# Kernel optimization log

Measured on AMD Instinct MI355X. Metric: run time of the kernel, lower is better.

Reference implementation:

```python
import jax, jax.numpy as jnp
import numpy as np
import math


def _conv2d(x, w, b):
    # 3x3, stride 1, pad 1, NCHW / OIHW
    y = jax.lax.conv_general_dilated(x, w, (1, 1), ((1, 1), (1, 1)),
                                     dimension_numbers=('NCHW', 'OIHW', 'NCHW'))
    return y + b[None, :, None, None]


def _avgpool2(x):
    B, C, H, W = x.shape
    return x.reshape(B, C, H // 2, 2, W // 2, 2).mean(axis=(3, 5))


def setup_inputs() -> dict:
    key = jax.random.key(0)
    ks = jax.random.split(key, 12)
    B, H, W = 8, 512, 512
    x = jax.random.uniform(ks[0], (B, 3, H, W), dtype=jnp.float32)

    def conv_w(k, o, i):
        return jax.random.normal(k, (o, i, 3, 3), jnp.float32) / jnp.sqrt(jnp.float32(i * 9))

    def lin_w(k, o, i):
        return jax.random.normal(k, (o, i), jnp.float32) / jnp.sqrt(jnp.float32(i))

    return {
        'x': x,
        'w1': conv_w(ks[1], 16, 6),  'b1': jnp.zeros((16,), jnp.float32),
        'w2': conv_w(ks[2], 32, 16), 'b2': jnp.zeros((32,), jnp.float32),
        'w3': conv_w(ks[3], 64, 32), 'b3': jnp.zeros((64,), jnp.float32),
        'fw1': lin_w(ks[4], 256, 64),  'fb1': jnp.zeros((256,), jnp.float32),
        'fw2': lin_w(ks[5], 100, 256), 'fb2': jnp.zeros((100,), jnp.float32),
    }


def reference(x, w1, b1, w2, b2, w3, b3, fw1, fb1, fw2, fb2):
    B, C, H, W = x.shape
    # radial distance from image center (torch.meshgrid default = 'ij')
    a, b = jnp.meshgrid(jnp.arange(H), jnp.arange(W), indexing='ij')
    dist = jnp.sqrt((a - H / 2) ** 2 + (b - W / 2) ** 2).astype(jnp.float32)
    max_radius = math.sqrt(H * H + W * W) / 2

    xf = jnp.fft.fftn(x, axes=(-1, -2))
    # torch.fft.fftshift with no dim shifts ALL axes (incl. B, C); jnp matches.
    xf = jnp.fft.fftshift(xf)
    x_mag = jnp.log10(jnp.abs(xf) + 1)

    fi = jnp.concatenate([x, x_mag], axis=1)  # [B,6,H,W]
    y = jax.nn.relu(_conv2d(fi, w1, b1))
    y = _avgpool2(y)
    y = jax.nn.relu(_conv2d(y, w2, b2))
    y = _avgpool2(y)
    y = _conv2d(y, w3, b3)
    y = y.mean(axis=(2, 3))  # AdaptiveAvgPool2d((1,1)) -> [B,64]
    # note: NO activation between the two FC layers in the original
    value_set = jax.nn.leaky_relu((y @ fw1.T + fb1) @ fw2.T + fb2, 0.01)  # [B,100]

    # 100 radial ring bins; replace the 100-iter where-loop with bucketize+gather
    radius_set = max_radius * (jnp.arange(100, dtype=jnp.float32) + 1.0) * 0.01
    # bin i: radius_set[i-1] < dist <= radius_set[i]  ==  searchsorted left
    bin_idx = jnp.clip(jnp.searchsorted(radius_set, dist, side='left'), 0, 99)  # [H,W]
    fq_mask = value_set[:, bin_idx]  # [B,H,W] gather, same math as sum of ring masks

    low = xf * fq_mask[:, None, :, :]
    low = jnp.fft.ifftshift(low)
    low = jnp.fft.ifftn(low, axes=(-1, -2))
    lowpass = jnp.clip(low.real, 0.0, 1.0)
    return lowpass, fq_mask, value_set
```

## Files before the change

kernel.cpp:

```cpp
#include <hip/hip_runtime.h>
#include <math.h>

#define NPIX 262144
#define FSTR 513

typedef __attribute__((ext_vector_type(2))) float v2f;


__device__ __forceinline__ int brev9(int i) { return (int)(__brev((unsigned)i) >> 23); }

__device__ __forceinline__ void wave_lds_fence() {
  asm volatile("s_waitcnt lgkmcnt(0)" ::: "memory");
}

__device__ __forceinline__ void init_tw(float* twr, float* twi, int t) {
  if (t < 256) {
    float ang = -3.14159265358979323846f * (float)t / 256.0f;
    float s, c;
    sincosf(ang, &s, &c);
    twr[t] = c; twi[t] = s;
  }
}

template<bool FWD>
__device__ __forceinline__ void fft512x8(float* __restrict__ sr, float* __restrict__ si,
                                         const float* __restrict__ twr,
                                         const float* __restrict__ twi, int t) {
  const int c  = t >> 5;
  const int tq = t & 31;
  float* cr = sr + c * FSTR;
  float* ci = si + c * FSTR;
  #pragma unroll
  for (int sp = 0; sp < 4; sp++) {
    const int s = 2 * sp;
    const int h = 1 << s;
    if (sp == 0) __syncthreads(); else wave_lds_fence();
    #pragma unroll
    for (int m = 0; m < 4; m++) {
      int q = tq + 32 * m;
      int j = q & (h - 1);
      int base = ((q >> s) << (s + 2)) | j;
      int i1 = j << (8 - s);
      int i2 = j << (7 - s);
      float w1r = twr[i1], w1i = FWD ? twi[i1] : -twi[i1];
      float w2r = twr[i2], w2i = FWD ? twi[i2] : -twi[i2];
      float ar = cr[base],         ai = ci[base];
      float br = cr[base + h],     bi = ci[base + h];
      float c2r = cr[base + 2*h],  c2i = ci[base + 2*h];
      float dr = cr[base + 3*h],   di = ci[base + 3*h];
      float wbr = br * w1r - bi * w1i, wbi = br * w1i + bi * w1r;
      float wdr = dr * w1r - di * w1i, wdi = dr * w1i + di * w1r;
      float t0r = ar + wbr,  t0i = ai + wbi;
      float t1r = ar - wbr,  t1i = ai - wbi;
      float t2r = c2r + wdr, t2i = c2i + wdi;
      float t3r = c2r - wdr, t3i = c2i - wdi;
      float u2r = t2r * w2r - t2i * w2i, u2i = t2r * w2i + t2i * w2r;
      float v3r = t3r * w2r - t3i * w2i, v3i = t3r * w2i + t3i * w2r;
      float u3r = FWD ? v3i : -v3i;
      float u3i = FWD ? -v3r : v3r;
      cr[base]         = t0r + u2r;  ci[base]         = t0i + u2i;
      cr[base + 2*h]   = t0r - u2r;  ci[base + 2*h]   = t0i - u2i;
      cr[base + h]     = t1r + u3r;  ci[base + h]     = t1i + u3i;
      cr[base + 3*h]   = t1r - u3r;  ci[base + 3*h]   = t1i - u3i;
    }
  }
  wave_lds_fence();
  #pragma unroll
  for (int m = 0; m < 8; m++) {
    int k = tq + 32 * m;
    float wr = twr[k], wi = FWD ? twi[k] : -twi[k];
    float vr = cr[k + 256], vi = ci[k + 256];
    float tr = vr * wr - vi * wi;
    float ti = vr * wi + vi * wr;
    float ur = cr[k], ui = ci[k];
    cr[k] = ur + tr;        ci[k] = ui + ti;
    cr[k + 256] = ur - tr;  ci[k + 256] = ui - ti;
  }
  __syncthreads();
}

__device__ __forceinline__ void pair_src(int p, int& ia, int& ib) {
  if (p < 8) { ia = 3 * p; ib = 3 * p + 1; }
  else { int k = p - 8; ia = 6 * k + 2; ib = 6 * k + 5; }
}

__global__ __launch_bounds__(256) void k_fft_rows(const float* __restrict__ x,
                                                  float2* __restrict__ xf) {
  __shared__ float sr[8 * FSTR], si[8 * FSTR], twr[256], twi[256];
  int t = threadIdx.x;
  int p = blockIdx.x >> 6;
  int r0 = (blockIdx.x & 63) << 3;
  init_tw(twr, twi, t);
  int ia, ib;
  pair_src(p, ia, ib);
  const float4* pa = (const float4*)(x + (size_t)ia * NPIX + (size_t)r0 * 512);
  const float4* pb = (const float4*)(x + (size_t)ib * NPIX + (size_t)r0 * 512);
  for (int e = t; e < 1024; e += 256) {
    int row = e >> 7, w = e & 127;
    float4 fa = pa[e];
    float4 fb = pb[e];
    float* cr = sr + row * FSTR;
    float* ci = si + row * FSTR;
    int pc = 4 * w;
    cr[brev9(pc)]     = fa.x;  ci[brev9(pc)]     = fb.x;
    cr[brev9(pc + 1)] = fa.y;  ci[brev9(pc + 1)] = fb.y;
    cr[brev9(pc + 2)] = fa.z;  ci[brev9(pc + 2)] = fb.z;
    cr[brev9(pc + 3)] = fa.w;  ci[brev9(pc + 3)] = fb.w;
  }
  fft512x8<true>(sr, si, twr, twi, t);
  float4* q4 = (float4*)(xf + (size_t)p * NPIX + (size_t)r0 * 512);
  for (int e = t; e < 2048; e += 256) {
    int row = e >> 8, u = e & 255;
    const float* cr = sr + row * FSTR;
    const float* ci = si + row * FSTR;
    q4[e] = make_float4(cr[2 * u], ci[2 * u], cr[2 * u + 1], ci[2 * u + 1]);
  }
}

__global__ __launch_bounds__(256) void k_fft_cols(float2* __restrict__ xf) {
  __shared__ float sr[8 * FSTR], si[8 * FSTR], twr[256], twi[256];
  int t = threadIdx.x;
  int p = blockIdx.x >> 6;
  int c0 = (blockIdx.x & 63) << 3;
  init_tw(twr, twi, t);
  float2* base = xf + (size_t)p * NPIX + c0;
  const int q = t & 3;
  const int j = (t >> 2) & 15;
  const int w = t >> 6;
  #pragma unroll
  for (int it = 0; it < 8; it++) {
    int row = 32 * j + 4 * it + w;
    float4 f = *(const float4*)(base + (size_t)row * 512 + 2 * q);
    int rr = brev9(row);
    sr[(2 * q) * FSTR + rr]     = f.x;  si[(2 * q) * FSTR + rr]     = f.y;
    sr[(2 * q + 1) * FSTR + rr] = f.z;  si[(2 * q + 1) * FSTR + rr] = f.w;
  }
  fft512x8<true>(sr, si, twr, twi, t);
  const int rg = t >> 2;
  #pragma unroll
  for (int it = 0; it < 8; it++) {
    int row = 64 * it + rg;
    float a0 = sr[(2 * q) * FSTR + row],     b0 = si[(2 * q) * FSTR + row];
    float a1 = sr[(2 * q + 1) * FSTR + row], b1 = si[(2 * q + 1) * FSTR + row];
    *(float4*)(base + (size_t)row * 512 + 2 * q) = make_float4(a0, b0, a1, b1);
  }
}

__global__ __launch_bounds__(256) void k_xmag(const float2* __restrict__ xf,
                                              float* __restrict__ xmag) {
  int t = threadIdx.x;
  int p = blockIdx.x >> 6;
  int r0 = (blockIdx.x & 63) << 3;
  int da, db;
  if (p < 8) {
    int bs = (p + 4) & 7;
    da = bs * 3 + 1;
    db = bs * 3 + 2;
  } else {
    int k = p - 8;
    da = ((2 * k + 4) & 7) * 3;
    db = ((2 * k + 5) & 7) * 3;
  }
  const float2* Z = xf + (size_t)p * NPIX;
  float* A = xmag + (size_t)da * NPIX;
  float* B = xmag + (size_t)db * NPIX;
  for (int e = t; e < 2048; e += 256) {
    int row = r0 + (e >> 8);
    int c0 = (e & 255) * 2;
    float4 z01 = *(const float4*)(Z + (size_t)row * 512 + c0);
    int mr = (512 - row) & 511;
    float2 zm0 = Z[(size_t)mr * 512 + ((512 - c0) & 511)];
    float2 zm1 = Z[(size_t)mr * 512 + (511 - c0)];
    float ar0 = 0.5f * (z01.x + zm0.x), ai0 = 0.5f * (z01.y - zm0.y);
    float br0 = 0.5f * (z01.x - zm0.x), bi0 = 0.5f * (z01.y + zm0.y);
    float ar1 = 0.5f * (z01.z + zm1.x), ai1 = 0.5f * (z01.w - zm1.y);
    float br1 = 0.5f * (z01.z - zm1.x), bi1 = 0.5f * (z01.w + zm1.y);
    float ma0 = log10f(sqrtf(ar0 * ar0 + ai0 * ai0) + 1.0f);
    float ma1 = log10f(sqrtf(ar1 * ar1 + ai1 * ai1) + 1.0f);
    float mb0 = log10f(sqrtf(br0 * br0 + bi0 * bi0) + 1.0f);
    float mb1 = log10f(sqrtf(br1 * br1 + bi1 * bi1) + 1.0f);
    size_t off = (size_t)(row ^ 256) * 512 + (c0 ^ 256);
    *(float2*)(A + off) = make_float2(ma0, ma1);
    *(float2*)(B + off) = make_float2(mb0, mb1);
  }
}

__global__ __launch_bounds__(256) void k_conv1(const float* __restrict__ x,
                                               const float* __restrict__ xmag,
                                               const float* __restrict__ w1,
                                               const float* __restrict__ b1,
                                               float* __restrict__ out) {
  __shared__ float tile[2][18 * 132 + 8];
  const int t = threadIdx.x;
  const int tx = t & 31, ty = t >> 5;
  const int PC0 = blockIdx.x * 64;
  const int PR0 = blockIdx.y * 8;
  const int b  = blockIdx.z >> 1;
  const int og = (blockIdx.z & 1) * 8;
  const int R0 = PR0 * 2 - 1;
  const int C0 = PC0 * 2 - 1;

  int li[10], gi[10];
  bool okf[10];
  #pragma unroll
  for (int k = 0; k < 10; k++) {
    int e = t + 256 * k;
    bool valid = e < 2340;
    int i = e / 130, j = e - i * 130;
    int rr = R0 + i, cc = C0 + j;
    bool ok = valid && ((unsigned)rr < 512u) && ((unsigned)cc < 512u);
    li[k] = valid ? (i * 132 + j) : (18 * 132);
    gi[k] = ok ? (rr * 512 + cc) : 0;
    okf[k] = ok;
  }

  v2f acc[8][4];
  #pragma unroll
  for (int o = 0; o < 8; o++)
    #pragma unroll
    for (int q = 0; q < 4; q++) acc[o][q] = (v2f){0.0f, 0.0f};

  const float* xb = x + (size_t)(b * 3) * NPIX;
  const float* mb = xmag + (size_t)(b * 3) * NPIX;

  float ld[10];
  #pragma unroll
  for (int k = 0; k < 10; k++) ld[k] = okf[k] ? xb[gi[k]] : 0.0f;
  #pragma unroll
  for (int k = 0; k < 10; k++) tile[0][li[k]] = ld[k];
  __syncthreads();

  for (int ic = 0; ic < 6; ic++) {
    if (ic < 5) {
      const float* sn = (ic + 1 < 3) ? (xb + (size_t)(ic + 1) * NPIX)
                                     : (mb + (size_t)(ic - 2) * NPIX);
      #pragma unroll
      for (int k = 0; k < 10; k++) ld[k] = okf[k] ? sn[gi[k]] : 0.0f;
    }
    const float* cur = tile[ic & 1];
    float patch[4][6];
    #pragma unroll
    for (int dy = 0; dy < 4; dy++) {
      const float* rp = cur + (2 * ty + dy) * 132 + 4 * tx;
      float4 f = *(const float4*)rp;
      float2 g = *(const float2*)(rp + 4);
      patch[dy][0] = f.x; patch[dy][1] = f.y; patch[dy][2] = f.z;
      patch[dy][3] = f.w; patch[dy][4] = g.x; patch[dy][5] = g.y;
    }
    v2f pr[4][5];
    #pragma unroll
    for (int dy = 0; dy < 4; dy++)
      #pragma unroll
      for (int s = 0; s < 5; s++)
        pr[dy][s] = (v2f){patch[dy][s], patch[dy][s + 1]};
    #pragma unroll
    for (int o = 0; o < 8; o++) {
      const float* wk = w1 + (size_t)((og + o) * 6 + ic) * 9;
      #pragma unroll
      for (int dy = 0; dy < 3; dy++)
        #pragma unroll
        for (int kc = 0; kc < 3; kc++) {
          float kw = wk[dy * 3 + kc];
          v2f wv = (v2f){kw, kw};
          acc[o][0] += wv * pr[dy][kc];
          acc[o][1] += wv * pr[dy][kc + 2];
          acc[o][2] += wv * pr[dy + 1][kc];
          acc[o][3] += wv * pr[dy + 1][kc + 2];
        }
    }
    if (ic < 5) {
      float* nxt = tile[(ic + 1) & 1];
      #pragma unroll
      for (int k = 0; k < 10; k++) nxt[li[k]] = ld[k];
      __syncthreads();
    }
  }
  #pragma unroll
  for (int o = 0; o < 8; o++) {
    float bias = b1[og + o];
    float p0 = fmaxf(acc[o][0].x + bias, 0.0f) + fmaxf(acc[o][0].y + bias, 0.0f)
             + fmaxf(acc[o][2].x + bias, 0.0f) + fmaxf(acc[o][2].y + bias, 0.0f);
    float p1 = fmaxf(acc[o][1].x + bias, 0.0f) + fmaxf(acc[o][1].y + bias, 0.0f)
             + fmaxf(acc[o][3].x + bias, 0.0f) + fmaxf(acc[o][3].y + bias, 0.0f);
    float2* q = (float2*)(out + ((size_t)(b * 16 + og + o) * 256 + PR0 + ty) * 256 + PC0 + 2 * tx);
    *q = make_float2(p0 * 0.25f, p1 * 0.25f);
  }
}

__global__ __launch_bounds__(256) void k_conv2(const float* __restrict__ in,
                                               const float* __restrict__ w2,
                                               const float* __restrict__ b2,
                                               float* __restrict__ S) {
  __shared__ float tile[2][18 * 68 + 8];
  __shared__ float wsum[4][8];
  const int t = threadIdx.x;
  const int tx = t & 31, ty = t >> 5;
  const int bx = blockIdx.x, by = blockIdx.y;
  const int PC0 = bx * 32;
  const int PR0 = by * 8;
  const int b  = blockIdx.z >> 2;
  const int og = (blockIdx.z & 3) * 8;
  const int R0 = PR0 * 2 - 1;
  const int C0 = PC0 * 2 - 1;

  int li[5], gi[5];
  bool okf[5];
  #pragma unroll
  for (int k = 0; k < 5; k++) {
    int e = t + 256 * k;
    bool valid = e < 1188;
    int i = e / 66, j = e - 66 * i;
    int rr = R0 + i, cc = C0 + j;
    bool ok = valid && ((unsigned)rr < 256u) && ((unsigned)cc < 256u);
    li[k] = valid ? (i * 68 + j) : (18 * 68);
    gi[k] = ok ? (rr * 256 + cc) : 0;
    okf[k] = ok;
  }

  v2f acc[8][2];
  #pragma unroll
  for (int o = 0; o < 8; o++) {
    acc[o][0] = (v2f){0.0f, 0.0f};
    acc[o][1] = (v2f){0.0f, 0.0f};
  }

  const float* inb = in + (size_t)(b * 16) * 65536;

  float ld[5];
  #pragma unroll
  for (int k = 0; k < 5; k++) ld[k] = okf[k] ? inb[gi[k]] : 0.0f;
  #pragma unroll
  for (int k = 0; k < 5; k++) tile[0][li[k]] = ld[k];
  __syncthreads();

  for (int ic = 0; ic < 16; ic++) {
    if (ic < 15) {
      const float* sn = inb + (size_t)(ic + 1) * 65536;
      #pragma unroll
      for (int k = 0; k < 5; k++) ld[k] = okf[k] ? sn[gi[k]] : 0.0f;
    }
    const float* cur = tile[ic & 1];
    float patch[4][4];
    #pragma unroll
    for (int dy = 0; dy < 4; dy++) {
      const float* rp = cur + (2 * ty + dy) * 68 + 2 * tx;
      float2 f0 = *(const float2*)rp;
      float2 f1 = *(const float2*)(rp + 2);
      patch[dy][0] = f0.x; patch[dy][1] = f0.y;
      patch[dy][2] = f1.x; patch[dy][3] = f1.y;
    }
    v2f pr[4][3];
    #pragma unroll
    for (int dy = 0; dy < 4; dy++) {
      pr[dy][0] = (v2f){patch[dy][0], patch[dy][1]};
      pr[dy][1] = (v2f){patch[dy][1], patch[dy][2]};
      pr[dy][2] = (v2f){patch[dy][2], patch[dy][3]};
    }
    #pragma unroll
    for (int o = 0; o < 8; o++) {
      const float* wk = w2 + (size_t)((og + o) * 16 + ic) * 9;
      #pragma unroll
      for (int dy = 0; dy < 3; dy++)
        #pragma unroll
        for (int kc = 0; kc < 3; kc++) {
          float kw = wk[dy * 3 + kc];
          v2f wv = (v2f){kw, kw};
          acc[o][0] += wv * pr[dy][kc];
          acc[o][1] += wv * pr[dy + 1][kc];
        }
    }
    if (ic < 15) {
      float* nxt = tile[(ic + 1) & 1];
      #pragma unroll
      for (int k = 0; k < 5; k++) nxt[li[k]] = ld[k];
      __syncthreads();
    }
  }

  const int lane = t & 63;
  const int wid = t >> 6;
  float* Sb0 = S + (size_t)(b * 32 + og) * 9;
  #pragma unroll
  for (int o = 0; o < 8; o++) {
    float bias = b2[og + o];
    float v = (fmaxf(acc[o][0].x + bias, 0.0f) + fmaxf(acc[o][0].y + bias, 0.0f)
             + fmaxf(acc[o][1].x + bias, 0.0f) + fmaxf(acc[o][1].y + bias, 0.0f)) * 0.25f;
    float* Sb = Sb0 + o * 9;
    float ts = v;
    #pragma unroll
    for (int off = 32; off > 0; off >>= 1) ts += __shfl_down(ts, off);
    if (lane == 0) wsum[wid][o] = ts;
    if (by == 0) {
      float e = (ty == 0) ? v : 0.0f;
      #pragma unroll
      for (int off = 32; off > 0; off >>= 1) e += __shfl_down(e, off);
      if (lane == 0) atomicAdd(&Sb[1], e);
    }
    if (by == 15) {
      float e = (ty == 7) ? v : 0.0f;
      #pragma unroll
      for (int off = 32; off > 0; off >>= 1) e += __shfl_down(e, off);
      if (lane == 0) atomicAdd(&Sb[2], e);
    }
    if (bx == 0 && tx == 0)  atomicAdd(&Sb[3], v);
    if (bx == 3 && tx == 31) atomicAdd(&Sb[4], v);
    if (bx == 0 && by == 0  && t == 0)   Sb[5] = v;
    if (bx == 3 && by == 0  && t == 31)  Sb[6] = v;
    if (bx == 0 && by == 15 && t == 224) Sb[7] = v;
    if (bx == 3 && by == 15 && t == 255) Sb[8] = v;
  }
  __syncthreads();
  if (t < 8)
    atomicAdd(&Sb0[t * 9], wsum[0][t] + wsum[1][t] + wsum[2][t] + wsum[3][t]);
}

__global__ __launch_bounds__(256) void k_fc(const float* __restrict__ S,
                                            const float* __restrict__ w3,
                                            const float* __restrict__ b3,
                                            const float* __restrict__ fw1,
                                            const float* __restrict__ fb1,
                                            const float* __restrict__ fw2,
                                            const float* __restrict__ fb2,
                                            float* __restrict__ vs_out) {
  __shared__ float Sp[2304];
  __shared__ float y[512];
  __shared__ float h1[2048];
  int t = threadIdx.x;
  for (int e = t; e < 2304; e += 256) {
    int cell = e / 9, k = e - 9 * cell;
    int dy = k / 3, dx = k - 3 * dy;
    const float* s = S + cell * 9;
    float v = s[0];
    if (dy == 0) v -= s[2];
    if (dy == 2) v -= s[1];
    if (dx == 0) v -= s[4];
    if (dx == 2) v -= s[3];
    if (dy == 0 && dx == 0) v += s[8];
    if (dy == 0 && dx == 2) v += s[7];
    if (dy == 2 && dx == 0) v += s[6];
    if (dy == 2 && dx == 2) v += s[5];
    Sp[e] = v;
  }
  __syncthreads();
  for (int e = t; e < 512; e += 256) {
    int b = e >> 6, o = e & 63;
    const float* wrow = w3 + (size_t)o * 288;
    const float* sp = Sp + b * 288;
    float s = 0.0f;
    #pragma unroll 4
    for (int k = 0; k < 288; k++) s += wrow[k] * sp[k];
    y[e] = b3[o] + s * (1.0f / 16384.0f);
  }
  __syncthreads();
  for (int e = t; e < 2048; e += 256) {
    int b = e >> 8, j = e & 255;
    float s = fb1[j];
    for (int k = 0; k < 64; k++) s += y[b * 64 + k] * fw1[j * 64 + k];
    h1[e] = s;
  }
  __syncthreads();
  for (int e = t; e < 800; e += 256) {
    int b = e / 100, i = e - 100 * b;
    float s = fb2[i];
    for (int j = 0; j < 256; j++) s += h1[b * 256 + j] * fw2[i * 256 + j];
    vs_out[e] = (s >= 0.0f) ? s : 0.01f * s;
  }
}

__global__ __launch_bounds__(256) void k_mask(const float* __restrict__ vs,
                                              float* __restrict__ fq_mask) {
  int idx = blockIdx.x * 256 + threadIdx.x;
  int h = idx >> 9, w = idx & 511;
  float da = (float)h - 256.0f, db = (float)w - 256.0f;
  float dist = sqrtf(da * da + db * db);
  int lo = 0, hi = 100;
  while (lo < hi) {
    int mid = (lo + hi) >> 1;
    float r = (362.03867196751236f * (float)(mid + 1)) * 0.01f;
    if (r < dist) lo = mid + 1; else hi = mid;
  }
  int bin = lo > 99 ? 99 : lo;
  #pragma unroll
  for (int b = 0; b < 8; b++)
    fq_mask[(size_t)b * NPIX + idx] = vs[b * 100 + bin];
}

__global__ __launch_bounds__(256) void k_ifft_rows_mod(const float2* __restrict__ xf,
                                                       float2* __restrict__ xf2,
                                                       const float* __restrict__ fq_mask) {
  __shared__ float sr[8 * FSTR], si[8 * FSTR], twr[256], twi[256];
  int t = threadIdx.x;
  int p = blockIdx.x >> 6;
  int r0 = (blockIdx.x & 63) << 3;
  init_tw(twr, twi, t);
  if (p < 8) {
    int bm = (p + 4) & 7;
    const float* mbase = fq_mask + (size_t)bm * NPIX;
    const float4* base4 = (const float4*)(xf + (size_t)p * NPIX + (size_t)r0 * 512);
    for (int e = t; e < 2048; e += 256) {
      int u = (e & 3) | (((e >> 2) & 15) << 3) | (((e >> 6) & 1) << 2) | (((e >> 7) & 1) << 7);
      int row = e >> 8;
      float4 f = base4[row * 256 + u];
      int p0 = 2 * u;
      const float* mrow = mbase + (size_t)((r0 + row + 256) & 511) * 512;
      float2 m = *(const float2*)(mrow + ((p0 + 256) & 511));
      int rr0 = brev9(p0);
      float* cr = sr + row * FSTR;
      float* ci = si + row * FSTR;
      cr[rr0]       = f.x * m.x;  ci[rr0]       = f.y * m.x;
      cr[rr0 + 256] = f.z * m.y;  ci[rr0 + 256] = f.w * m.y;
    }
  } else {
    int k = p - 8;
    const float* fa = fq_mask + (size_t)((2 * k + 4) & 7) * NPIX;
    const float* fb = fq_mask + (size_t)((2 * k + 5) & 7) * NPIX;
    const float2* Z = xf + (size_t)p * NPIX;
    for (int e = t; e < 2048; e += 256) {
      int row = e >> 8;
      int gr = r0 + row;
      int c0 = (e & 255) * 2;
      float4 z01 = *(const float4*)(Z + (size_t)gr * 512 + c0);
      int mr = (512 - gr) & 511;
      float2 zm0 = Z[(size_t)mr * 512 + ((512 - c0) & 511)];
      float2 zm1 = Z[(size_t)mr * 512 + (511 - c0)];
      size_t mro = (size_t)((gr + 256) & 511) * 512;
      int mc = (c0 + 256) & 511;
      float2 ma = *(const float2*)(fa + mro + mc);
      float2 mb = *(const float2*)(fb + mro + mc);
      float s0 = 0.5f * (ma.x + mb.x), d0 = 0.5f * (ma.x - mb.x);
      float s1 = 0.5f * (ma.y + mb.y), d1 = 0.5f * (ma.y - mb.y);
      float wr0 = s0 * z01.x + d0 * zm0.x;
      float wi0 = s0 * z01.y - d0 * zm0.y;
      float wr1 = s1 * z01.z + d1 * zm1.x;
      float wi1 = s1 * z01.w - d1 * zm1.y;
      int rr0 = brev9(c0);
      float* cr = sr + row * FSTR;
      float* ci = si + row * FSTR;
      cr[rr0]       = wr0;  ci[rr0]       = wi0;
      cr[rr0 + 256] = wr1;  ci[rr0 + 256] = wi1;
    }
  }
  fft512x8<false>(sr, si, twr, twi, t);
  float4* o4 = (float4*)(xf2 + (size_t)p * NPIX + (size_t)r0 * 512);
  for (int e = t; e < 2048; e += 256) {
    int row = e >> 8, u = e & 255;
    const float* cr = sr + row * FSTR;
    const float* ci = si + row * FSTR;
    o4[e] = make_float4(cr[2 * u], ci[2 * u], cr[2 * u + 1], ci[2 * u + 1]);
  }
}

__global__ __launch_bounds__(256) void k_ifft_cols_out(const float2* __restrict__ xf2,
                                                       float* __restrict__ lowpass) {
  __shared__ float sr[8 * FSTR], si[8 * FSTR], twr[256], twi[256];
  int t = threadIdx.x;
  int p = blockIdx.x >> 6;
  int c0 = (blockIdx.x & 63) << 3;
  init_tw(twr, twi, t);
  const float2* base = xf2 + (size_t)p * NPIX + c0;
  const int q = t & 3;
  const int j = (t >> 2) & 15;
  const int w = t >> 6;
  #pragma unroll
  for (int it = 0; it < 8; it++) {
    int row = 32 * j + 4 * it + w;
    float4 f = *(const float4*)(base + (size_t)row * 512 + 2 * q);
    int rr = brev9(row);
    sr[(2 * q) * FSTR + rr]     = f.x;  si[(2 * q) * FSTR + rr]     = f.y;
    sr[(2 * q + 1) * FSTR + rr] = f.z;  si[(2 * q + 1) * FSTR + rr] = f.w;
  }
  fft512x8<false>(sr, si, twr, twi, t);
  const float sc = 1.0f / 262144.0f;
  int ia, ib;
  pair_src(p, ia, ib);
  float* oa = lowpass + (size_t)ia * NPIX + c0;
  float* ob = lowpass + (size_t)ib * NPIX + c0;
  const int rg = t >> 2;
  #pragma unroll
  for (int it = 0; it < 8; it++) {
    int row = 64 * it + rg;
    float re0 = sr[(2 * q) * FSTR + row],     im0 = si[(2 * q) * FSTR + row];
    float re1 = sr[(2 * q + 1) * FSTR + row], im1 = si[(2 * q + 1) * FSTR + row];
    float a0 = fminf(fmaxf(re0 * sc, 0.0f), 1.0f);
    float a1 = fminf(fmaxf(re1 * sc, 0.0f), 1.0f);
    float b0 = fminf(fmaxf(im0 * sc, 0.0f), 1.0f);
    float b1 = fminf(fmaxf(im1 * sc, 0.0f), 1.0f);
    *(float2*)(oa + (size_t)row * 512 + 2 * q) = make_float2(a0, a1);
    *(float2*)(ob + (size_t)row * 512 + 2 * q) = make_float2(b0, b1);
  }
}

extern "C" void kernel_launch(void* const* d_in, const int* in_sizes, int n_in,
                              void* d_out, int out_size, void* d_ws, size_t ws_size,
                              hipStream_t stream) {
  const float* x   = (const float*)d_in[0];
  const float* w1  = (const float*)d_in[1];
  const float* b1  = (const float*)d_in[2];
  const float* w2  = (const float*)d_in[3];
  const float* b2  = (const float*)d_in[4];
  const float* w3  = (const float*)d_in[5];
  const float* b3  = (const float*)d_in[6];
  const float* fw1 = (const float*)d_in[7];
  const float* fb1 = (const float*)d_in[8];
  const float* fw2 = (const float*)d_in[9];
  const float* fb2 = (const float*)d_in[10];

  float* lowpass = (float*)d_out;
  float* fq_mask = lowpass + 6291456;
  float* vs      = fq_mask + 2097152;

  float* base    = (float*)d_ws;
  float2* xf     = (float2*)base;
  float2* xf2    = (float2*)(base + 6291456);
  float* xmag    = base + 12582912;
  float* pooled1 = xmag + 6291456;
  float* S       = pooled1 + 8388608;

  k_fft_rows<<<dim3(12 * 64), 256, 0, stream>>>(x, xf);
  k_fft_cols<<<dim3(12 * 64), 256, 0, stream>>>(xf);
  k_xmag<<<dim3(12 * 64), 256, 0, stream>>>(xf, xmag);

  k_conv1<<<dim3(4, 32, 16), 256, 0, stream>>>(x, xmag, w1, b1, pooled1);
  hipMemsetAsync(S, 0, 2304 * sizeof(float), stream);
  k_conv2<<<dim3(4, 16, 32), 256, 0, stream>>>(pooled1, w2, b2, S);

  k_fc<<<1, 256, 0, stream>>>(S, w3, b3, fw1, fb1, fw2, fb2, vs);
  k_mask<<<1024, 256, 0, stream>>>(vs, fq_mask);

  k_ifft_rows_mod<<<dim3(12 * 64), 256, 0, stream>>>(xf, xf2, fq_mask);
  k_ifft_cols_out<<<dim3(12 * 64), 256, 0, stream>>>(xf2, lowpass);
}
```

Before: 358.1 us.

## Pad pooled1 planes with zero halo and stage conv2 tiles via global_load_lds

conv1 now writes its pooled output into padded 258x260 planes and zeroes the halo borders itself. conv2 can therefore load its input tile with unconditional direct global-to-LDS loads (global_load_lds), skipping the bounds checks and the register round-trip. The LDS tile is made dense (row stride 66), and xmag is aliased onto the xf2 workspace region to make room. In exchange, conv2's LDS reads now use an unpadded stride that may cause bank conflicts. Correctness also depends on every halo cell being zeroed and on the new workspace aliasing being safe.

```diff
diff --git a/kernel.cpp b/kernel.cpp
--- a/kernel.cpp
+++ b/kernel.cpp
@@ -3,6 +3,7 @@
 
 #define NPIX 262144
 #define FSTR 513
+#define PPLANE 67080
 
 typedef __attribute__((ext_vector_type(2))) float v2f;
 
@@ -11,6 +12,13 @@
 
 __device__ __forceinline__ void wave_lds_fence() {
   asm volatile("s_waitcnt lgkmcnt(0)" ::: "memory");
+}
+
+__device__ __forceinline__ void gload_lds4(const float* __restrict__ gsrc,
+                                           float* __restrict__ ldst) {
+  __builtin_amdgcn_global_load_lds(
+      (const __attribute__((address_space(1))) void*)gsrc,
+      (__attribute__((address_space(3))) void*)ldst, 4, 0, 0);
 }
 
 __device__ __forceinline__ void init_tw(float* twr, float* twi, int t) {
@@ -193,12 +201,35 @@
   __shared__ float tile[2][18 * 132 + 8];
   const int t = threadIdx.x;
   const int tx = t & 31, ty = t >> 5;
-  const int PC0 = blockIdx.x * 64;
-  const int PR0 = blockIdx.y * 8;
+  const int bx1 = blockIdx.x, by1 = blockIdx.y;
+  const int PC0 = bx1 * 64;
+  const int PR0 = by1 * 8;
   const int b  = blockIdx.z >> 1;
   const int og = (blockIdx.z & 1) * 8;
   const int R0 = PR0 * 2 - 1;
   const int C0 = PC0 * 2 - 1;
+
+  if (by1 == 0 || by1 == 31) {
+    int row = (by1 == 0) ? 0 : 257;
+    int sc = PC0 + 2, len = 64;
+    if (bx1 == 0) { sc = 1; len = 65; }
+    if (bx1 == 3) { len += 1; }
+    #pragma unroll 1
+    for (int o = 0; o < 8; o++) {
+      float* pl = out + (size_t)(b * 16 + og + o) * PPLANE + (size_t)row * 260;
+      for (int e = t; e < len; e += 256) pl[sc + e] = 0.0f;
+    }
+  }
+  if (bx1 == 0 || bx1 == 3) {
+    int col = (bx1 == 0) ? 1 : 258;
+    if (t < 8) {
+      #pragma unroll 1
+      for (int o = 0; o < 8; o++) {
+        float* pl = out + (size_t)(b * 16 + og + o) * PPLANE + col;
+        pl[(size_t)(PR0 + 1 + t) * 260] = 0.0f;
+      }
+    }
+  }
 
   int li[10], gi[10];
   bool okf[10];
@@ -282,7 +313,8 @@
              + fmaxf(acc[o][2].x + bias, 0.0f) + fmaxf(acc[o][2].y + bias, 0.0f);
     float p1 = fmaxf(acc[o][1].x + bias, 0.0f) + fmaxf(acc[o][1].y + bias, 0.0f)
              + fmaxf(acc[o][3].x + bias, 0.0f) + fmaxf(acc[o][3].y + bias, 0.0f);
-    float2* q = (float2*)(out + ((size_t)(b * 16 + og + o) * 256 + PR0 + ty) * 256 + PC0 + 2 * tx);
+    float2* q = (float2*)(out + (size_t)(b * 16 + og + o) * PPLANE
+                              + (size_t)(PR0 + ty + 1) * 260 + PC0 + 2 * tx + 2);
     *q = make_float2(p0 * 0.25f, p1 * 0.25f);
   }
 }
@@ -291,7 +323,7 @@
                                                const float* __restrict__ w2,
                                                const float* __restrict__ b2,
                                                float* __restrict__ S) {
-  __shared__ float tile[2][18 * 68 + 8];
+  __shared__ float tile[2][1216];
   __shared__ float wsum[4][8];
   const int t = threadIdx.x;
   const int tx = t & 31, ty = t >> 5;
@@ -303,18 +335,13 @@
   const int R0 = PR0 * 2 - 1;
   const int C0 = PC0 * 2 - 1;
 
-  int li[5], gi[5];
-  bool okf[5];
+  int gi[5];
   #pragma unroll
   for (int k = 0; k < 5; k++) {
     int e = t + 256 * k;
-    bool valid = e < 1188;
+    if (e > 1187) e = 1187;
     int i = e / 66, j = e - 66 * i;
-    int rr = R0 + i, cc = C0 + j;
-    bool ok = valid && ((unsigned)rr < 256u) && ((unsigned)cc < 256u);
-    li[k] = valid ? (i * 68 + j) : (18 * 68);
-    gi[k] = ok ? (rr * 256 + cc) : 0;
-    okf[k] = ok;
+    gi[k] = (R0 + i + 1) * 260 + (C0 + j + 2);
   }
 
   v2f acc[8][2];
@@ -324,26 +351,23 @@
     acc[o][1] = (v2f){0.0f, 0.0f};
   }
 
-  const float* inb = in + (size_t)(b * 16) * 65536;
-
-  float ld[5];
-  #pragma unroll
-  for (int k = 0; k < 5; k++) ld[k] = okf[k] ? inb[gi[k]] : 0.0f;
-  #pragma unroll
-  for (int k = 0; k < 5; k++) tile[0][li[k]] = ld[k];
-  __syncthreads();
-
-  for (int ic = 0; ic < 16; ic++) {
-    if (ic < 15) {
-      const float* sn = inb + (size_t)(ic + 1) * 65536;
-      #pragma unroll
-      for (int k = 0; k < 5; k++) ld[k] = okf[k] ? sn[gi[k]] : 0.0f;
-    }
-    const float* cur = tile[ic & 1];
+  const float* inb = in + (size_t)(b * 16) * PPLANE;
+  const int wbase = t & 192;
+
+  auto STAGE = [&](int bsel, int ic) {
+    const float* sp = inb + (size_t)ic * PPLANE;
+    #pragma unroll
+    for (int k = 0; k < 5; k++) {
+      if (k < 4 || t < 192)
+        gload_lds4(sp + gi[k], &tile[bsel][wbase + 256 * k]);
+    }
+  };
+  auto COMPUTE = [&](int bsel, int ic) {
+    const float* cur = tile[bsel];
     float patch[4][4];
     #pragma unroll
     for (int dy = 0; dy < 4; dy++) {
-      const float* rp = cur + (2 * ty + dy) * 68 + 2 * tx;
+      const float* rp = cur + (2 * ty + dy) * 66 + 2 * tx;
       float2 f0 = *(const float2*)rp;
       float2 f1 = *(const float2*)(rp + 2);
       patch[dy][0] = f0.x; patch[dy][1] = f0.y;
@@ -369,12 +393,15 @@
           acc[o][1] += wv * pr[dy + 1][kc];
         }
     }
-    if (ic < 15) {
-      float* nxt = tile[(ic + 1) & 1];
-      #pragma unroll
-      for (int k = 0; k < 5; k++) nxt[li[k]] = ld[k];
-      __syncthreads();
-    }
+  };
+
+  STAGE(0, 0);
+  __syncthreads();
+
+  for (int ic = 0; ic < 16; ic++) {
+    if (ic < 15) STAGE((ic + 1) & 1, ic + 1);
+    COMPUTE(ic & 1, ic);
+    if (ic < 15) __syncthreads();
   }
 
   const int lane = t & 63;
@@ -611,10 +638,10 @@
 
   float* base    = (float*)d_ws;
   float2* xf     = (float2*)base;
+  float* xmag    = base + 6291456;
   float2* xf2    = (float2*)(base + 6291456);
-  float* xmag    = base + 12582912;
-  float* pooled1 = xmag + 6291456;
-  float* S       = pooled1 + 8388608;
+  float* pooled1 = base + 12582912;
+  float* S       = pooled1 + 8586240;
 
   k_fft_rows<<<dim3(12 * 64), 256, 0, stream>>>(x, xf);
   k_fft_cols<<<dim3(12 * 64), 256, 0, stream>>>(xf);
```

Measured after the change: 361.4 us. About the same (+0.9%).
